# Kernel tuning notes

Measured on AMD Instinct MI355X. Metric: run time of the kernel, lower is better.

## Reference

```python
import jax, jax.numpy as jnp
import numpy as np

N = 100000   # num nodes
D = 256      # latent_dim
B = 4096     # batch nodes
K = 32       # max padded degree per view
NREL = 9     # relation types 0..8
TEMP = 0.07

VIEW1_RELS = np.array([0, 7, 8])
VIEW2_RELS = np.array([1, 2, 3, 4, 5, 6])


def setup_inputs() -> dict:
    key = jax.random.key(0)
    ks = jax.random.split(key, 16)
    inv_sqrt_d = 1.0 / np.sqrt(D)
    node_features = jax.random.normal(ks[0], (N, D), dtype=jnp.float32)
    rel_emb = jax.random.normal(ks[1], (NREL, D), dtype=jnp.float32) * 0.1
    nb_ids1 = jax.random.randint(ks[2], (B, K), 0, N)
    nb_ids2 = jax.random.randint(ks[3], (B, K), 0, N)
    rel_ids1 = jnp.asarray(VIEW1_RELS)[jax.random.randint(ks[4], (B, K), 0, len(VIEW1_RELS))]
    rel_ids2 = jnp.asarray(VIEW2_RELS)[jax.random.randint(ks[5], (B, K), 0, len(VIEW2_RELS))]
    mask1 = jax.random.randint(ks[6], (B, K), 0, 2).astype(bool)
    mask2 = jax.random.randint(ks[7], (B, K), 0, 2).astype(bool)
    batch_node_ids = jax.random.randint(ks[8], (B,), 0, N)
    W1a = jax.random.normal(ks[9], (D, D), dtype=jnp.float32) * inv_sqrt_d
    b1a = jnp.zeros((D,), dtype=jnp.float32)
    W1b = jax.random.normal(ks[10], (D, D // 2), dtype=jnp.float32) * inv_sqrt_d
    b1b = jnp.zeros((D // 2,), dtype=jnp.float32)
    W2a = jax.random.normal(ks[11], (D, D), dtype=jnp.float32) * inv_sqrt_d
    b2a = jnp.zeros((D,), dtype=jnp.float32)
    W2b = jax.random.normal(ks[12], (D, D // 2), dtype=jnp.float32) * inv_sqrt_d
    b2b = jnp.zeros((D // 2,), dtype=jnp.float32)
    return dict(node_features=node_features, rel_emb=rel_emb,
                nb_ids1=nb_ids1, rel_ids1=rel_ids1, mask1=mask1,
                nb_ids2=nb_ids2, rel_ids2=rel_ids2, mask2=mask2,
                batch_node_ids=batch_node_ids,
                W1a=W1a, b1a=b1a, W1b=W1b, b1b=b1b,
                W2a=W2a, b2a=b2a, W2b=W2b, b2b=b2b)


def _aggregate(nf, rel_emb, nb_ids, rel_ids, mask, self_ids):
    # [B,K,D] messages = neighbor feature + relation embedding
    msg = nf[nb_ids] + rel_emb[rel_ids]
    m = mask[..., None].astype(nf.dtype)
    cnt = mask.sum(axis=-1).astype(nf.dtype)            # [B]
    mean = (msg * m).sum(axis=1) / jnp.maximum(cnt, 1.0)[:, None]
    # nodes with no neighbors fall back to their own feature
    return jnp.where((cnt > 0)[:, None], mean, nf[self_ids])


def _proj(x, Wa, ba, Wb, bb):
    h = jax.nn.relu(x @ Wa + ba)
    return h @ Wb + bb


def _infonce(z1, z2, temperature):
    z1 = z1 / jnp.linalg.norm(z1, axis=-1, keepdims=True)
    z2 = z2 / jnp.linalg.norm(z2, axis=-1, keepdims=True)
    sim = (z1 @ z2.T) / temperature                      # [B,B]
    lsm12 = jax.nn.log_softmax(sim, axis=-1)
    lsm21 = jax.nn.log_softmax(sim.T, axis=-1)
    diag = jnp.arange(sim.shape[0])
    loss_12 = -lsm12[diag, diag].mean()
    loss_21 = -lsm21[diag, diag].mean()
    return (loss_12 + loss_21) / 2


def reference(node_features, rel_emb, nb_ids1, rel_ids1, mask1,
              nb_ids2, rel_ids2, mask2, batch_node_ids,
              W1a, b1a, W1b, b1b, W2a, b2a, W2b, b2b):
    v1 = _aggregate(node_features, rel_emb, nb_ids1, rel_ids1, mask1, batch_node_ids)
    v2 = _aggregate(node_features, rel_emb, nb_ids2, rel_ids2, mask2, batch_node_ids)
    z1 = _proj(v1, W1a, b1a, W1b, b1b)
    z2 = _proj(v2, W2a, b2a, W2b, b2b)
    return _infonce(z1, z2, TEMP)
```

## Files before the change

kernel.cpp:

```cpp
#include <hip/hip_runtime.h>
#include <hip/hip_bf16.h>
#include <math.h>

#define NN 100000
#define DD 256
#define BB 4096
#define KK 32
#define ZD 128
#define INVTEMP (1.0f/0.07f)

typedef unsigned short u16;
typedef __attribute__((ext_vector_type(8))) short short8;
typedef __attribute__((ext_vector_type(4))) float floatx4;

__device__ inline u16 f2bf(float f) {
  __hip_bfloat16 h = __float2bfloat16(f);
  return *reinterpret_cast<u16*>(&h);
}

__global__ void convw_kernel(const float* __restrict__ W, u16* __restrict__ Wt, int N) {
  int idx = blockIdx.x * 256 + threadIdx.x;
  int n = idx >> 8;
  int k = idx & 255;
  Wt[idx] = f2bf(W[k * N + n]);
}

__global__ void aggregate_kernel(const float* __restrict__ nf,
                                 const float* __restrict__ rel,
                                 const int* __restrict__ nb1, const int* __restrict__ rl1, const int* __restrict__ mk1,
                                 const int* __restrict__ nb2, const int* __restrict__ rl2, const int* __restrict__ mk2,
                                 const int* __restrict__ self_ids,
                                 u16* __restrict__ v1, u16* __restrict__ v2) {
  int b = blockIdx.x;
  const int *nb, *rl, *mk;
  u16* out;
  if (blockIdx.y == 0) { nb = nb1; rl = rl1; mk = mk1; out = v1; }
  else                 { nb = nb2; rl = rl2; mk = mk2; out = v2; }
  int tid = threadIdx.x;
  int g = tid >> 6, c = tid & 63;

  float ax = 0.f, ay = 0.f, az = 0.f, aw = 0.f;
  int cnt = 0;
#pragma unroll
  for (int kk = 0; kk < 8; ++kk) {
    int k = kk * 4 + g;
    if (mk[b * KK + k]) {
      int nid = nb[b * KK + k];
      int rid = rl[b * KK + k];
      float4 m = *(const float4*)(nf + (size_t)nid * DD + c * 4);
      float4 r = *(const float4*)(rel + (size_t)rid * DD + c * 4);
      ax += m.x + r.x; ay += m.y + r.y; az += m.z + r.z; aw += m.w + r.w;
      cnt++;
    }
  }
  __shared__ float sbuf[4][64][4];
  __shared__ int scnt[4];
  sbuf[g][c][0] = ax; sbuf[g][c][1] = ay; sbuf[g][c][2] = az; sbuf[g][c][3] = aw;
  if (c == 0) scnt[g] = cnt;
  __syncthreads();
  if (g == 0) {
    float sx = sbuf[0][c][0] + sbuf[1][c][0] + sbuf[2][c][0] + sbuf[3][c][0];
    float sy = sbuf[0][c][1] + sbuf[1][c][1] + sbuf[2][c][1] + sbuf[3][c][1];
    float sz = sbuf[0][c][2] + sbuf[1][c][2] + sbuf[2][c][2] + sbuf[3][c][2];
    float sw = sbuf[0][c][3] + sbuf[1][c][3] + sbuf[2][c][3] + sbuf[3][c][3];
    int tot = scnt[0] + scnt[1] + scnt[2] + scnt[3];
    float rx, ry, rz, rw;
    if (tot > 0) {
      float inv = 1.0f / (float)tot;
      rx = sx * inv; ry = sy * inv; rz = sz * inv; rw = sw * inv;
    } else {
      float4 s = *(const float4*)(nf + (size_t)self_ids[b] * DD + c * 4);
      rx = s.x; ry = s.y; rz = s.z; rw = s.w;
    }
    union { u16 us[4]; uint2 u2; } pk;
    pk.us[0] = f2bf(rx); pk.us[1] = f2bf(ry); pk.us[2] = f2bf(rz); pk.us[3] = f2bf(rw);
    *(uint2*)(out + (size_t)b * DD + c * 4) = pk.u2;
  }
}

template<int RELU, int OUTBF16>
__global__ void mfma_gemm_bt(const u16* __restrict__ A, const u16* __restrict__ Bt,
                             const float* __restrict__ bias, void* __restrict__ C,
                             int M, int N, int K) {
  int tid = threadIdx.x;
  int lane = tid & 63, wid = tid >> 6;
  int m16 = lane & 15, q = lane >> 4;
  int rowbase = blockIdx.x * 128 + (wid >> 1) * 64;
  int colbase = blockIdx.y * 128 + (wid & 1) * 64;
  floatx4 acc[4][4] = {};
  for (int k0 = 0; k0 < K; k0 += 32) {
    short8 a[4], b[4];
#pragma unroll
    for (int i = 0; i < 4; i++)
      a[i] = *(const short8*)(A + (size_t)(rowbase + i * 16 + m16) * K + k0 + q * 8);
#pragma unroll
    for (int j = 0; j < 4; j++)
      b[j] = *(const short8*)(Bt + (size_t)(colbase + j * 16 + m16) * K + k0 + q * 8);
#pragma unroll
    for (int i = 0; i < 4; i++)
#pragma unroll
      for (int j = 0; j < 4; j++)
        acc[i][j] = __builtin_amdgcn_mfma_f32_16x16x32_bf16(a[i], b[j], acc[i][j], 0, 0, 0);
  }
#pragma unroll
  for (int i = 0; i < 4; i++) {
#pragma unroll
    for (int j = 0; j < 4; j++) {
      int col = colbase + j * 16 + m16;
      float bv = bias[col];
#pragma unroll
      for (int r = 0; r < 4; r++) {
        int row = rowbase + i * 16 + q * 4 + r;
        float v = acc[i][j][r] + bv;
        if (RELU) v = fmaxf(v, 0.f);
        if (OUTBF16) ((u16*)C)[(size_t)row * N + col] = f2bf(v);
        else         ((float*)C)[(size_t)row * N + col] = v;
      }
    }
  }
}

__global__ void normalize_diag(const float* __restrict__ z1f, const float* __restrict__ z2f,
                               u16* __restrict__ z1, u16* __restrict__ z2,
                               float* __restrict__ diag) {
  int i = blockIdx.x, t = threadIdx.x;
  float2 a = *(const float2*)(z1f + (size_t)i * ZD + t * 2);
  float2 b = *(const float2*)(z2f + (size_t)i * ZD + t * 2);
  float s1 = a.x * a.x + a.y * a.y;
  float s2 = b.x * b.x + b.y * b.y;
#pragma unroll
  for (int off = 1; off < 64; off <<= 1) {
    s1 += __shfl_xor(s1, off);
    s2 += __shfl_xor(s2, off);
  }
  float n1 = rsqrtf(s1), n2 = rsqrtf(s2);
  float ax = a.x * n1, ay = a.y * n1;
  float bx = b.x * n2, by = b.y * n2;
  union { u16 us[2]; unsigned u; } p1, p2;
  p1.us[0] = f2bf(ax); p1.us[1] = f2bf(ay);
  p2.us[0] = f2bf(bx); p2.us[1] = f2bf(by);
  *(unsigned*)(z1 + (size_t)i * ZD + t * 2) = p1.u;
  *(unsigned*)(z2 + (size_t)i * ZD + t * 2) = p2.u;
  float d = ax * bx + ay * by;
#pragma unroll
  for (int off = 1; off < 64; off <<= 1) d += __shfl_xor(d, off);
  if (t == 0) diag[i] = d * INVTEMP;
}

__global__ void sim_kernel(const u16* __restrict__ z1, const u16* __restrict__ z2,
                           float* __restrict__ rowsum, float* __restrict__ colsum) {
  int tid = threadIdx.x;
  int lane = tid & 63, wid = tid >> 6;
  int m16 = lane & 15, q = lane >> 4;
  int rowbase = blockIdx.x * 128 + (wid >> 1) * 64;
  int colbase = blockIdx.y * 128 + (wid & 1) * 64;
  floatx4 acc[4][4] = {};
  for (int k0 = 0; k0 < ZD; k0 += 32) {
    short8 a[4], b[4];
#pragma unroll
    for (int i = 0; i < 4; i++)
      a[i] = *(const short8*)(z1 + (size_t)(rowbase + i * 16 + m16) * ZD + k0 + q * 8);
#pragma unroll
    for (int j = 0; j < 4; j++)
      b[j] = *(const short8*)(z2 + (size_t)(colbase + j * 16 + m16) * ZD + k0 + q * 8);
#pragma unroll
    for (int i = 0; i < 4; i++)
#pragma unroll
      for (int j = 0; j < 4; j++)
        acc[i][j] = __builtin_amdgcn_mfma_f32_16x16x32_bf16(a[i], b[j], acc[i][j], 0, 0, 0);
  }
  float rowacc[4][4] = {};
  float colacc[4] = {};
#pragma unroll
  for (int i = 0; i < 4; i++)
#pragma unroll
    for (int j = 0; j < 4; j++)
#pragma unroll
      for (int r = 0; r < 4; r++) {
        float e = __expf(acc[i][j][r] * INVTEMP);
        rowacc[i][r] += e;
        colacc[j] += e;
      }
#pragma unroll
  for (int off = 1; off <= 8; off <<= 1)
#pragma unroll
    for (int i = 0; i < 4; i++)
#pragma unroll
      for (int r = 0; r < 4; r++) rowacc[i][r] += __shfl_xor(rowacc[i][r], off);
  if (m16 == 0) {
#pragma unroll
    for (int i = 0; i < 4; i++)
#pragma unroll
      for (int r = 0; r < 4; r++)
        atomicAdd(&rowsum[rowbase + i * 16 + q * 4 + r], rowacc[i][r]);
  }
#pragma unroll
  for (int off = 16; off <= 32; off <<= 1)
#pragma unroll
    for (int j = 0; j < 4; j++) colacc[j] += __shfl_xor(colacc[j], off);
  if (q == 0) {
#pragma unroll
    for (int j = 0; j < 4; j++)
      atomicAdd(&colsum[colbase + j * 16 + m16], colacc[j]);
  }
}

__global__ void loss_kernel(const float* __restrict__ rowsum, const float* __restrict__ colsum,
                            const float* __restrict__ diag, float* __restrict__ out) {
  int tid = threadIdx.x;
  float acc = 0.f;
  for (int i = tid; i < BB; i += 256)
    acc += 0.5f * (logf(rowsum[i]) + logf(colsum[i])) - diag[i];
#pragma unroll
  for (int off = 1; off < 64; off <<= 1) acc += __shfl_xor(acc, off);
  __shared__ float sbuf[4];
  if ((tid & 63) == 0) sbuf[tid >> 6] = acc;
  __syncthreads();
  if (tid == 0) out[0] = (sbuf[0] + sbuf[1] + sbuf[2] + sbuf[3]) * (1.0f / BB);
}

extern "C" void kernel_launch(void* const* d_in, const int* in_sizes, int n_in,
                              void* d_out, int out_size, void* d_ws, size_t ws_size,
                              hipStream_t stream) {
  const float* nf  = (const float*)d_in[0];
  const float* rel = (const float*)d_in[1];
  const int* nb1 = (const int*)d_in[2];
  const int* rl1 = (const int*)d_in[3];
  const int* mk1 = (const int*)d_in[4];
  const int* nb2 = (const int*)d_in[5];
  const int* rl2 = (const int*)d_in[6];
  const int* mk2 = (const int*)d_in[7];
  const int* self_ids = (const int*)d_in[8];
  const float* W1a = (const float*)d_in[9];
  const float* b1a = (const float*)d_in[10];
  const float* W1b = (const float*)d_in[11];
  const float* b1b = (const float*)d_in[12];
  const float* W2a = (const float*)d_in[13];
  const float* b2a = (const float*)d_in[14];
  const float* W2b = (const float*)d_in[15];
  const float* b2b = (const float*)d_in[16];

  char* ws = (char*)d_ws;
  u16* v1   = (u16*)ws;                 ws += (size_t)BB * DD * 2;
  u16* v2   = (u16*)ws;                 ws += (size_t)BB * DD * 2;
  u16* h1   = (u16*)ws;                 ws += (size_t)BB * DD * 2;
  u16* h2   = (u16*)ws;                 ws += (size_t)BB * DD * 2;
  float* z1f = (float*)ws;              ws += (size_t)BB * ZD * 4;
  float* z2f = (float*)ws;              ws += (size_t)BB * ZD * 4;
  u16* z1   = (u16*)ws;                 ws += (size_t)BB * ZD * 2;
  u16* z2   = (u16*)ws;                 ws += (size_t)BB * ZD * 2;
  u16* W1at = (u16*)ws;                 ws += (size_t)DD * DD * 2;
  u16* W2at = (u16*)ws;                 ws += (size_t)DD * DD * 2;
  u16* W1bt = (u16*)ws;                 ws += (size_t)ZD * DD * 2;
  u16* W2bt = (u16*)ws;                 ws += (size_t)ZD * DD * 2;
  float* rowsum = (float*)ws;           ws += (size_t)BB * 4;
  float* colsum = (float*)ws;           ws += (size_t)BB * 4;
  float* diag   = (float*)ws;           ws += (size_t)BB * 4;

  convw_kernel<<<DD, 256, 0, stream>>>(W1a, W1at, DD);
  convw_kernel<<<DD, 256, 0, stream>>>(W2a, W2at, DD);
  convw_kernel<<<ZD, 256, 0, stream>>>(W1b, W1bt, ZD);
  convw_kernel<<<ZD, 256, 0, stream>>>(W2b, W2bt, ZD);

  aggregate_kernel<<<dim3(BB, 2), 256, 0, stream>>>(nf, rel, nb1, rl1, mk1,
                                                    nb2, rl2, mk2, self_ids, v1, v2);

  mfma_gemm_bt<1, 1><<<dim3(BB / 128, DD / 128), 256, 0, stream>>>(v1, W1at, b1a, h1, BB, DD, DD);
  mfma_gemm_bt<1, 1><<<dim3(BB / 128, DD / 128), 256, 0, stream>>>(v2, W2at, b2a, h2, BB, DD, DD);
  mfma_gemm_bt<0, 0><<<dim3(BB / 128, ZD / 128), 256, 0, stream>>>(h1, W1bt, b1b, z1f, BB, ZD, DD);
  mfma_gemm_bt<0, 0><<<dim3(BB / 128, ZD / 128), 256, 0, stream>>>(h2, W2bt, b2b, z2f, BB, ZD, DD);

  normalize_diag<<<BB, 64, 0, stream>>>(z1f, z2f, z1, z2, diag);

  hipMemsetAsync(rowsum, 0, 2 * (size_t)BB * sizeof(float), stream);
  sim_kernel<<<dim3(BB / 128, BB / 128), 256, 0, stream>>>(z1, z2, rowsum, colsum);
  loss_kernel<<<1, 256, 0, stream>>>(rowsum, colsum, diag, (float*)d_out);
}
```

Measured before the change: 293.7 us.

## Fuse projection GEMMs through shared memory and merge small launches

Merges the four weight-conversion launches into one kernel. Fuses both layers of each projection MLP into a single kernel that keeps the hidden activation in padded LDS instead of writing it to global memory. Folds the rowsum/colsum memset into normalize_diag and adds launch bounds to the sim kernel. This cuts launch count and the round trip of h1/h2 through global memory, but the fused projection now runs only 64 blocks with one block per CU, which lowers parallelism.

```diff
diff --git a/kernel.cpp b/kernel.cpp
--- a/kernel.cpp
+++ b/kernel.cpp
@@ -8,6 +8,7 @@
 #define KK 32
 #define ZD 128
 #define INVTEMP (1.0f/0.07f)
+#define HS 264
 
 typedef unsigned short u16;
 typedef __attribute__((ext_vector_type(8))) short short8;
@@ -18,11 +19,18 @@
   return *reinterpret_cast<u16*>(&h);
 }
 
-__global__ void convw_kernel(const float* __restrict__ W, u16* __restrict__ Wt, int N) {
+__global__ void convw_all(const float* __restrict__ W1a, const float* __restrict__ W2a,
+                          const float* __restrict__ W1b, const float* __restrict__ W2b,
+                          u16* __restrict__ W1at, u16* __restrict__ W2at,
+                          u16* __restrict__ W1bt, u16* __restrict__ W2bt) {
   int idx = blockIdx.x * 256 + threadIdx.x;
-  int n = idx >> 8;
-  int k = idx & 255;
-  Wt[idx] = f2bf(W[k * N + n]);
+  const float* W; u16* Wt; int N, off;
+  if (idx < 65536)       { W = W1a; Wt = W1at; N = 256; off = idx; }
+  else if (idx < 131072) { W = W2a; Wt = W2at; N = 256; off = idx - 65536; }
+  else if (idx < 163840) { W = W1b; Wt = W1bt; N = 128; off = idx - 131072; }
+  else                   { W = W2b; Wt = W2bt; N = 128; off = idx - 163840; }
+  int n = off >> 8, k = off & 255;
+  Wt[off] = f2bf(W[k * N + n]);
 }
 
 __global__ void aggregate_kernel(const float* __restrict__ nf,
@@ -78,52 +86,96 @@
   }
 }
 
-template<int RELU, int OUTBF16>
-__global__ void mfma_gemm_bt(const u16* __restrict__ A, const u16* __restrict__ Bt,
-                             const float* __restrict__ bias, void* __restrict__ C,
-                             int M, int N, int K) {
+__global__ void __launch_bounds__(256, 1)
+proj_fused(const u16* __restrict__ v1, const u16* __restrict__ v2,
+           const u16* __restrict__ W1at, const u16* __restrict__ W2at,
+           const float* __restrict__ b1a, const float* __restrict__ b2a,
+           const u16* __restrict__ W1bt, const u16* __restrict__ W2bt,
+           const float* __restrict__ b1b, const float* __restrict__ b2b,
+           float* __restrict__ z1f, float* __restrict__ z2f) {
+  const u16 *v, *Wat, *Wbt;
+  const float *ba, *bb;
+  float* zf;
+  if (blockIdx.y == 0) { v = v1; Wat = W1at; ba = b1a; Wbt = W1bt; bb = b1b; zf = z1f; }
+  else                 { v = v2; Wat = W2at; ba = b2a; Wbt = W2bt; bb = b2b; zf = z2f; }
+  __shared__ u16 hs[128 * HS];
   int tid = threadIdx.x;
   int lane = tid & 63, wid = tid >> 6;
   int m16 = lane & 15, q = lane >> 4;
-  int rowbase = blockIdx.x * 128 + (wid >> 1) * 64;
-  int colbase = blockIdx.y * 128 + (wid & 1) * 64;
-  floatx4 acc[4][4] = {};
-  for (int k0 = 0; k0 < K; k0 += 32) {
-    short8 a[4], b[4];
-#pragma unroll
-    for (int i = 0; i < 4; i++)
-      a[i] = *(const short8*)(A + (size_t)(rowbase + i * 16 + m16) * K + k0 + q * 8);
-#pragma unroll
-    for (int j = 0; j < 4; j++)
-      b[j] = *(const short8*)(Bt + (size_t)(colbase + j * 16 + m16) * K + k0 + q * 8);
-#pragma unroll
-    for (int i = 0; i < 4; i++)
+  int rh = wid >> 1, ch = wid & 1;
+  int M0 = blockIdx.x * 128;
+  int rowl = rh * 64;
+
+  for (int nt = 0; nt < 2; ++nt) {
+    int colb = nt * 128 + ch * 64;
+    floatx4 acc[4][4] = {};
+    for (int k0 = 0; k0 < DD; k0 += 32) {
+      short8 a[4], b[4];
+#pragma unroll
+      for (int i = 0; i < 4; i++)
+        a[i] = *(const short8*)(v + (size_t)(M0 + rowl + i * 16 + m16) * DD + k0 + q * 8);
 #pragma unroll
       for (int j = 0; j < 4; j++)
-        acc[i][j] = __builtin_amdgcn_mfma_f32_16x16x32_bf16(a[i], b[j], acc[i][j], 0, 0, 0);
-  }
-#pragma unroll
-  for (int i = 0; i < 4; i++) {
-#pragma unroll
-    for (int j = 0; j < 4; j++) {
-      int col = colbase + j * 16 + m16;
-      float bv = bias[col];
-#pragma unroll
-      for (int r = 0; r < 4; r++) {
-        int row = rowbase + i * 16 + q * 4 + r;
-        float v = acc[i][j][r] + bv;
-        if (RELU) v = fmaxf(v, 0.f);
-        if (OUTBF16) ((u16*)C)[(size_t)row * N + col] = f2bf(v);
-        else         ((float*)C)[(size_t)row * N + col] = v;
+        b[j] = *(const short8*)(Wat + (size_t)(colb + j * 16 + m16) * DD + k0 + q * 8);
+#pragma unroll
+      for (int i = 0; i < 4; i++)
+#pragma unroll
+        for (int j = 0; j < 4; j++)
+          acc[i][j] = __builtin_amdgcn_mfma_f32_16x16x32_bf16(a[i], b[j], acc[i][j], 0, 0, 0);
+    }
+#pragma unroll
+    for (int i = 0; i < 4; i++)
+#pragma unroll
+      for (int j = 0; j < 4; j++) {
+        int col = colb + j * 16 + m16;
+        float bv = ba[col];
+#pragma unroll
+        for (int r = 0; r < 4; r++) {
+          int row = rowl + i * 16 + q * 4 + r;
+          hs[row * HS + col] = f2bf(fmaxf(acc[i][j][r] + bv, 0.f));
+        }
       }
+  }
+  __syncthreads();
+
+  {
+    int colb = ch * 64;
+    floatx4 acc[4][4] = {};
+    for (int k0 = 0; k0 < DD; k0 += 32) {
+      short8 a[4], b[4];
+#pragma unroll
+      for (int i = 0; i < 4; i++)
+        a[i] = *(const short8*)(hs + (rowl + i * 16 + m16) * HS + k0 + q * 8);
+#pragma unroll
+      for (int j = 0; j < 4; j++)
+        b[j] = *(const short8*)(Wbt + (size_t)(colb + j * 16 + m16) * DD + k0 + q * 8);
+#pragma unroll
+      for (int i = 0; i < 4; i++)
+#pragma unroll
+        for (int j = 0; j < 4; j++)
+          acc[i][j] = __builtin_amdgcn_mfma_f32_16x16x32_bf16(a[i], b[j], acc[i][j], 0, 0, 0);
     }
+#pragma unroll
+    for (int i = 0; i < 4; i++)
+#pragma unroll
+      for (int j = 0; j < 4; j++) {
+        int col = colb + j * 16 + m16;
+        float bv = bb[col];
+#pragma unroll
+        for (int r = 0; r < 4; r++) {
+          int row = M0 + rowl + i * 16 + q * 4 + r;
+          zf[(size_t)row * ZD + col] = acc[i][j][r] + bv;
+        }
+      }
   }
 }
 
 __global__ void normalize_diag(const float* __restrict__ z1f, const float* __restrict__ z2f,
                                u16* __restrict__ z1, u16* __restrict__ z2,
-                               float* __restrict__ diag) {
+                               float* __restrict__ diag,
+                               float* __restrict__ rowsum, float* __restrict__ colsum) {
   int i = blockIdx.x, t = threadIdx.x;
+  if (t == 0) { rowsum[i] = 0.f; colsum[i] = 0.f; }
   float2 a = *(const float2*)(z1f + (size_t)i * ZD + t * 2);
   float2 b = *(const float2*)(z2f + (size_t)i * ZD + t * 2);
   float s1 = a.x * a.x + a.y * a.y;
@@ -147,8 +199,9 @@
   if (t == 0) diag[i] = d * INVTEMP;
 }
 
-__global__ void sim_kernel(const u16* __restrict__ z1, const u16* __restrict__ z2,
-                           float* __restrict__ rowsum, float* __restrict__ colsum) {
+__global__ void __launch_bounds__(256, 2)
+sim_kernel(const u16* __restrict__ z1, const u16* __restrict__ z2,
+           float* __restrict__ rowsum, float* __restrict__ colsum) {
   int tid = threadIdx.x;
   int lane = tid & 63, wid = tid >> 6;
   int m16 = lane & 15, q = lane >> 4;
@@ -243,8 +296,6 @@
   char* ws = (char*)d_ws;
   u16* v1   = (u16*)ws;                 ws += (size_t)BB * DD * 2;
   u16* v2   = (u16*)ws;                 ws += (size_t)BB * DD * 2;
-  u16* h1   = (u16*)ws;                 ws += (size_t)BB * DD * 2;
-  u16* h2   = (u16*)ws;                 ws += (size_t)BB * DD * 2;
   float* z1f = (float*)ws;              ws += (size_t)BB * ZD * 4;
   float* z2f = (float*)ws;              ws += (size_t)BB * ZD * 4;
   u16* z1   = (u16*)ws;                 ws += (size_t)BB * ZD * 2;
@@ -257,22 +308,12 @@
   float* colsum = (float*)ws;           ws += (size_t)BB * 4;
   float* diag   = (float*)ws;           ws += (size_t)BB * 4;
 
-  convw_kernel<<<DD, 256, 0, stream>>>(W1a, W1at, DD);
-  convw_kernel<<<DD, 256, 0, stream>>>(W2a, W2at, DD);
-  convw_kernel<<<ZD, 256, 0, stream>>>(W1b, W1bt, ZD);
-  convw_kernel<<<ZD, 256, 0, stream>>>(W2b, W2bt, ZD);
-
+  convw_all<<<768, 256, 0, stream>>>(W1a, W2a, W1b, W2b, W1at, W2at, W1bt, W2bt);
   aggregate_kernel<<<dim3(BB, 2), 256, 0, stream>>>(nf, rel, nb1, rl1, mk1,
                                                     nb2, rl2, mk2, self_ids, v1, v2);
-
-  mfma_gemm_bt<1, 1><<<dim3(BB / 128, DD / 128), 256, 0, stream>>>(v1, W1at, b1a, h1, BB, DD, DD);
-  mfma_gemm_bt<1, 1><<<dim3(BB / 128, DD / 128), 256, 0, stream>>>(v2, W2at, b2a, h2, BB, DD, DD);
-  mfma_gemm_bt<0, 0><<<dim3(BB / 128, ZD / 128), 256, 0, stream>>>(h1, W1bt, b1b, z1f, BB, ZD, DD);
-  mfma_gemm_bt<0, 0><<<dim3(BB / 128, ZD / 128), 256, 0, stream>>>(h2, W2bt, b2b, z2f, BB, ZD, DD);
-
-  normalize_diag<<<BB, 64, 0, stream>>>(z1f, z2f, z1, z2, diag);
-
-  hipMemsetAsync(rowsum, 0, 2 * (size_t)BB * sizeof(float), stream);
+  proj_fused<<<dim3(BB / 128, 2), 256, 0, stream>>>(v1, v2, W1at, W2at, b1a, b2a,
+                                                    W1bt, W2bt, b1b, b2b, z1f, z2f);
+  normalize_diag<<<BB, 64, 0, stream>>>(z1f, z2f, z1, z2, diag, rowsum, colsum);
   sim_kernel<<<dim3(BB / 128, BB / 128), 256, 0, stream>>>(z1, z2, rowsum, colsum);
   loss_kernel<<<1, 256, 0, stream>>>(rowsum, colsum, diag, (float*)d_out);
 }
```

New measurement: 255.3 us. 13.1% less time.
